# Performance work log

Hardware: AMD Instinct MI355X
Metric: run time of the kernel (lower is better)

Reference implementation:

```python
import jax, jax.numpy as jnp
import numpy as np

B, K, D = 262144, 512, 3


def setup_inputs() -> dict:
    key = jax.random.key(0)
    k_ze, k_e = jax.random.split(key)
    ze = jax.random.normal(k_ze, (B, D, 1), dtype=jnp.float32)
    e = jax.random.normal(k_e, (K, D), dtype=jnp.float32)  # codebook, learned param
    return {"ze": ze, "e": e}


def reference(ze, e):
    # ze: (B, D, 1), e: (K, D)
    # Per-dimension L2 distance to every codebook entry: (B, K, D)
    l2diff = (jnp.transpose(ze, (0, 2, 1)) - e[None, :, :]) ** 2
    # Independent argmin over the codebook axis for each of the D dims: (B, D)
    z = jnp.argmin(l2diff, axis=1)
    # Gather per-dimension codebook scalars: zq[b, d] = e[z[b, d], d]
    zq = e[z, jnp.arange(D)]  # (B, D)
    return (z, zq)
```

## Files before the change

### kernel.cpp

```cpp
#include <hip/hip_runtime.h>

#define B_TOTAL 262144
#define K_CB    512
#define D_DIM   3
#define BLOCK   256
#define NSLOT   (B_TOTAL * D_DIM)

__device__ __forceinline__ unsigned int mono32(unsigned int u) {
    unsigned int m = (u & 0x80000000u) ? 0xFFFFFFFFu : 0x80000000u;
    return u ^ m;
}

__global__ __launch_bounds__(BLOCK) void rank_kernel(
    const float* __restrict__ e, float* __restrict__ ws_val, int* __restrict__ ws_idx)
{
    const int d    = blockIdx.x >> 1;
    const int half = blockIdx.x & 1;
    const int tid  = threadIdx.x;

    __shared__ unsigned long long key[K_CB];
    __shared__ float              val[K_CB];

    for (int k = tid; k < K_CB; k += BLOCK) {
        float v = e[k * D_DIM + d];
        key[k] = ((unsigned long long)mono32(__float_as_uint(v)) << 32) | (unsigned int)k;
        val[k] = v;
    }
    __syncthreads();

    const int i = half * BLOCK + tid;
    const unsigned long long mykey = key[i];
    int rank = 0;
    #pragma unroll 8
    for (int j = 0; j < K_CB; ++j)
        rank += (key[j] < mykey) ? 1 : 0;

    ws_val[d * K_CB + rank] = val[i];
    ws_idx[d * K_CB + rank] = i;
}

__global__ __launch_bounds__(BLOCK) void vq_search_kernel(
    const float* __restrict__ ze,
    const float* __restrict__ ws_val, const int* __restrict__ ws_idx,
    float* __restrict__ z_out, float* __restrict__ zq_out)
{
    __shared__ float sval[D_DIM * K_CB];
    __shared__ int   sidx[D_DIM * K_CB];

    const int tid = threadIdx.x;
    {
        const float4* gv = (const float4*)ws_val; float4* lv = (float4*)sval;
        for (int i = tid; i < D_DIM * K_CB / 4; i += BLOCK) lv[i] = gv[i];
        const int4*   gi = (const int4*)ws_idx;   int4*   li = (int4*)sidx;
        for (int i = tid; i < D_DIM * K_CB / 4; i += BLOCK) li[i] = gi[i];
    }
    __syncthreads();

    const int s4 = (blockIdx.x * BLOCK + tid) * 4;
    const float4 xv4 = *(const float4*)(ze + s4);
    const float xs[4] = { xv4.x, xv4.y, xv4.z, xv4.w };

    const int d0 = s4 % 3;
    int dcur = d0;
    float zz[4], zq[4];

    #pragma unroll
    for (int q = 0; q < 4; ++q) {
        const int base = dcur * K_CB;
        dcur = (dcur == 2) ? 0 : dcur + 1;
        const float xv = xs[q];

        int lo = -1, hi = K_CB;
        #pragma unroll
        for (int it = 0; it < 10; ++it) {
            int mid = (lo + hi) >> 1;
            bool le = sval[base + mid] <= xv;
            lo = le ? mid : lo;
            hi = le ? hi : mid;
        }

        float dl = 3.402823466e38f, vl = 0.0f; int il = 0;
        if (lo >= 0) {
            vl = sval[base + lo];
            int p = lo;
            while (p > 0 && sval[base + p - 1] == vl) --p;
            il = sidx[base + p];
            float t = xv - vl;
            dl = t * t;
        }
        float dr = 3.402823466e38f, vr = 0.0f; int ir = 0;
        if (lo < K_CB - 1) {
            vr = sval[base + lo + 1];
            ir = sidx[base + lo + 1];
            float t = xv - vr;
            dr = t * t;
        }

        const bool pickR = (dr < dl) || ((dr == dl) && (ir < il));
        zz[q] = (float)(pickR ? ir : il);
        zq[q] = pickR ? vr : vl;
    }

    *(float4*)(z_out  + s4) = make_float4(zz[0], zz[1], zz[2], zz[3]);
    *(float4*)(zq_out + s4) = make_float4(zq[0], zq[1], zq[2], zq[3]);
}

extern "C" void kernel_launch(void* const* d_in, const int* in_sizes, int n_in,
                              void* d_out, int out_size, void* d_ws, size_t ws_size,
                              hipStream_t stream) {
    const float* ze = (const float*)d_in[0];
    const float* e  = (const float*)d_in[1];
    float* z_out  = (float*)d_out;
    float* zq_out = z_out + (size_t)NSLOT;

    float* ws_val = (float*)d_ws;
    int*   ws_idx = (int*)(ws_val + D_DIM * K_CB);

    rank_kernel     <<<D_DIM * 2,         BLOCK, 0, stream>>>(e, ws_val, ws_idx);
    vq_search_kernel<<<NSLOT / (4 * BLOCK), BLOCK, 0, stream>>>(ze, ws_val, ws_idx,
                                                                z_out, zq_out);
}
```

Baseline: 72.00 us.

## Add bucket lookup table to narrow codebook binary search range

The rank kernel now also builds, per dimension, a 1024-bucket lookup table over [-4,4) that gives how many sorted codebook entries fall below each bucket boundary. The search kernel loads this table into shared memory and uses it to bracket each query, running 4 bisection steps when the bracket is small and falling back to the full 10-step search otherwise. This cuts shared-memory lookups per element, at the cost of loading about 6 KB of extra LUT per block and some divergence on the fallback branch.

```diff
diff --git a/kernel.cpp b/kernel.cpp
--- a/kernel.cpp
+++ b/kernel.cpp
@@ -5,14 +5,22 @@
 #define D_DIM   3
 #define BLOCK   256
 #define NSLOT   (B_TOTAL * D_DIM)
+#define LUT_S   1032
 
 __device__ __forceinline__ unsigned int mono32(unsigned int u) {
     unsigned int m = (u & 0x80000000u) ? 0xFFFFFFFFu : 0x80000000u;
     return u ^ m;
 }
 
-__global__ __launch_bounds__(BLOCK) void rank_kernel(
-    const float* __restrict__ e, float* __restrict__ ws_val, int* __restrict__ ws_idx)
+__device__ __forceinline__ int bucket_of(float x) {
+    float tf = floorf((x + 4.0f) * 128.0f);
+    tf = fminf(fmaxf(tf, 0.0f), 1023.0f);
+    return (int)tf;
+}
+
+__global__ __launch_bounds__(BLOCK) void rank_lut_kernel(
+    const float* __restrict__ e, float* __restrict__ ws_val,
+    int* __restrict__ ws_idx, unsigned short* __restrict__ ws_lut)
 {
     const int d    = blockIdx.x >> 1;
     const int half = blockIdx.x & 1;
@@ -20,11 +28,14 @@
 
     __shared__ unsigned long long key[K_CB];
     __shared__ float              val[K_CB];
+    __shared__ int                bkt[K_CB];
 
     for (int k = tid; k < K_CB; k += BLOCK) {
         float v = e[k * D_DIM + d];
-        key[k] = ((unsigned long long)mono32(__float_as_uint(v)) << 32) | (unsigned int)k;
+        key[k] = ((unsigned long long)mono32(__float_as_uint(v)) << 32)
+               | (unsigned int)k;
         val[k] = v;
+        bkt[k] = bucket_of(v);
     }
     __syncthreads();
 
@@ -37,15 +48,31 @@
 
     ws_val[d * K_CB + rank] = val[i];
     ws_idx[d * K_CB + rank] = i;
+
+    const int i0 = half * 512 + tid;
+    const int i1 = i0 + BLOCK;
+    int c0 = 0, c1 = 0;
+    #pragma unroll 8
+    for (int j = 0; j < K_CB; ++j) {
+        int bj = bkt[j];
+        c0 += (bj < i0) ? 1 : 0;
+        c1 += (bj < i1) ? 1 : 0;
+    }
+    ws_lut[d * LUT_S + i0] = (unsigned short)c0;
+    ws_lut[d * LUT_S + i1] = (unsigned short)c1;
+    if (half == 1 && tid == 0)
+        ws_lut[d * LUT_S + 1024] = (unsigned short)K_CB;
 }
 
 __global__ __launch_bounds__(BLOCK) void vq_search_kernel(
     const float* __restrict__ ze,
     const float* __restrict__ ws_val, const int* __restrict__ ws_idx,
+    const unsigned int* __restrict__ ws_lut_u32,
     float* __restrict__ z_out, float* __restrict__ zq_out)
 {
-    __shared__ float sval[D_DIM * K_CB];
-    __shared__ int   sidx[D_DIM * K_CB];
+    __shared__ __align__(16) float          sval[D_DIM * K_CB];
+    __shared__ __align__(16) int            sidx[D_DIM * K_CB];
+    __shared__ __align__(4)  unsigned short slut[D_DIM * LUT_S];
 
     const int tid = threadIdx.x;
     {
@@ -53,6 +80,8 @@
         for (int i = tid; i < D_DIM * K_CB / 4; i += BLOCK) lv[i] = gv[i];
         const int4*   gi = (const int4*)ws_idx;   int4*   li = (int4*)sidx;
         for (int i = tid; i < D_DIM * K_CB / 4; i += BLOCK) li[i] = gi[i];
+        unsigned int* ll = (unsigned int*)slut;
+        for (int i = tid; i < D_DIM * LUT_S / 2; i += BLOCK) ll[i] = ws_lut_u32[i];
     }
     __syncthreads();
 
@@ -60,23 +89,37 @@
     const float4 xv4 = *(const float4*)(ze + s4);
     const float xs[4] = { xv4.x, xv4.y, xv4.z, xv4.w };
 
-    const int d0 = s4 % 3;
-    int dcur = d0;
+    int dcur = s4 % 3;
     float zz[4], zq[4];
 
     #pragma unroll
     for (int q = 0; q < 4; ++q) {
         const int base = dcur * K_CB;
+        const int lutb = dcur * LUT_S;
         dcur = (dcur == 2) ? 0 : dcur + 1;
         const float xv = xs[q];
 
-        int lo = -1, hi = K_CB;
-        #pragma unroll
-        for (int it = 0; it < 10; ++it) {
-            int mid = (lo + hi) >> 1;
-            bool le = sval[base + mid] <= xv;
-            lo = le ? mid : lo;
-            hi = le ? hi : mid;
+        const int t  = bucket_of(xv);
+        int lo = (int)slut[lutb + t] - 1;
+        int hi = (int)slut[lutb + t + 1];
+
+        if (hi - lo > 16) {
+            lo = -1; hi = K_CB;
+            #pragma unroll
+            for (int it = 0; it < 10; ++it) {
+                int mid = (lo + hi) >> 1;
+                bool le = sval[base + mid] <= xv;
+                lo = le ? mid : lo;
+                hi = le ? hi : mid;
+            }
+        } else {
+            #pragma unroll
+            for (int it = 0; it < 4; ++it) {
+                int mid = (lo + hi) >> 1;
+                bool le = sval[base + mid] <= xv;
+                lo = le ? mid : lo;
+                hi = le ? hi : mid;
+            }
         }
 
         float dl = 3.402823466e38f, vl = 0.0f; int il = 0;
@@ -85,15 +128,15 @@
             int p = lo;
             while (p > 0 && sval[base + p - 1] == vl) --p;
             il = sidx[base + p];
-            float t = xv - vl;
-            dl = t * t;
+            float tt = xv - vl;
+            dl = tt * tt;
         }
         float dr = 3.402823466e38f, vr = 0.0f; int ir = 0;
         if (lo < K_CB - 1) {
             vr = sval[base + lo + 1];
             ir = sidx[base + lo + 1];
-            float t = xv - vr;
-            dr = t * t;
+            float tt = xv - vr;
+            dr = tt * tt;
         }
 
         const bool pickR = (dr < dl) || ((dr == dl) && (ir < il));
@@ -113,10 +156,11 @@
     float* z_out  = (float*)d_out;
     float* zq_out = z_out + (size_t)NSLOT;
 
-    float* ws_val = (float*)d_ws;
-    int*   ws_idx = (int*)(ws_val + D_DIM * K_CB);
+    float*          ws_val = (float*)d_ws;
+    int*            ws_idx = (int*)(ws_val + D_DIM * K_CB);
+    unsigned short* ws_lut = (unsigned short*)(ws_idx + D_DIM * K_CB);
 
-    rank_kernel     <<<D_DIM * 2,         BLOCK, 0, stream>>>(e, ws_val, ws_idx);
-    vq_search_kernel<<<NSLOT / (4 * BLOCK), BLOCK, 0, stream>>>(ze, ws_val, ws_idx,
-                                                                z_out, zq_out);
+    rank_lut_kernel <<<D_DIM * 2,           BLOCK, 0, stream>>>(e, ws_val, ws_idx, ws_lut);
+    vq_search_kernel<<<NSLOT / (4 * BLOCK), BLOCK, 0, stream>>>(
+        ze, ws_val, ws_idx, (const unsigned int*)ws_lut, z_out, zq_out);
 }
```

After: 77.72 us. 8.0% more time.

## Fuse codebook ranking and search into one cooperative kernel with grid sync

Applied to the files above, without the earlier changes.

Merges the small codebook-sorting kernel and the main search kernel into one cooperative launch. The first six blocks compute the sorted codebook, then every block waits at a grid-wide barrier before loading the sorted table into shared memory. This removes one kernel launch and the gap between the two kernels. In exchange it adds a grid barrier across 768 blocks and the extra cost of a cooperative launch, and it requires every block to be resident at the same time.

```diff
diff --git a/kernel.cpp b/kernel.cpp
--- a/kernel.cpp
+++ b/kernel.cpp
@@ -1,53 +1,59 @@
 #include <hip/hip_runtime.h>
+#include <hip/hip_cooperative_groups.h>
+
+namespace cg = cooperative_groups;
 
 #define B_TOTAL 262144
 #define K_CB    512
 #define D_DIM   3
 #define BLOCK   256
 #define NSLOT   (B_TOTAL * D_DIM)
+#define NBLK    (NSLOT / (4 * BLOCK))
 
 __device__ __forceinline__ unsigned int mono32(unsigned int u) {
     unsigned int m = (u & 0x80000000u) ? 0xFFFFFFFFu : 0x80000000u;
     return u ^ m;
 }
 
-__global__ __launch_bounds__(BLOCK) void rank_kernel(
-    const float* __restrict__ e, float* __restrict__ ws_val, int* __restrict__ ws_idx)
-{
-    const int d    = blockIdx.x >> 1;
-    const int half = blockIdx.x & 1;
-    const int tid  = threadIdx.x;
-
-    __shared__ unsigned long long key[K_CB];
-    __shared__ float              val[K_CB];
-
-    for (int k = tid; k < K_CB; k += BLOCK) {
-        float v = e[k * D_DIM + d];
-        key[k] = ((unsigned long long)mono32(__float_as_uint(v)) << 32) | (unsigned int)k;
-        val[k] = v;
-    }
-    __syncthreads();
-
-    const int i = half * BLOCK + tid;
-    const unsigned long long mykey = key[i];
-    int rank = 0;
-    #pragma unroll 8
-    for (int j = 0; j < K_CB; ++j)
-        rank += (key[j] < mykey) ? 1 : 0;
-
-    ws_val[d * K_CB + rank] = val[i];
-    ws_idx[d * K_CB + rank] = i;
-}
-
-__global__ __launch_bounds__(BLOCK) void vq_search_kernel(
-    const float* __restrict__ ze,
-    const float* __restrict__ ws_val, const int* __restrict__ ws_idx,
+__global__ __launch_bounds__(BLOCK) void vq_coop_kernel(
+    const float* __restrict__ ze, const float* __restrict__ e,
+    float* __restrict__ ws_val, int* __restrict__ ws_idx,
     float* __restrict__ z_out, float* __restrict__ zq_out)
 {
-    __shared__ float sval[D_DIM * K_CB];
-    __shared__ int   sidx[D_DIM * K_CB];
+    __shared__ __align__(16) unsigned char smem[12288];
+    const int tid = threadIdx.x;
 
-    const int tid = threadIdx.x;
+    if (blockIdx.x < D_DIM * 2) {
+        unsigned long long* key = (unsigned long long*)smem;
+        float*              val = (float*)(smem + 8192);
+
+        const int d    = blockIdx.x >> 1;
+        const int half = blockIdx.x & 1;
+
+        for (int k = tid; k < K_CB; k += BLOCK) {
+            float v = e[k * D_DIM + d];
+            key[k] = ((unsigned long long)mono32(__float_as_uint(v)) << 32)
+                   | (unsigned int)k;
+            val[k] = v;
+        }
+        __syncthreads();
+
+        const int i = half * BLOCK + tid;
+        const unsigned long long mykey = key[i];
+        int rank = 0;
+        #pragma unroll 8
+        for (int j = 0; j < K_CB; ++j)
+            rank += (key[j] < mykey) ? 1 : 0;
+
+        ws_val[d * K_CB + rank] = val[i];
+        ws_idx[d * K_CB + rank] = i;
+    }
+
+    cg::this_grid().sync();
+
+    float* sval = (float*)smem;
+    int*   sidx = (int*)(smem + 6144);
+
     {
         const float4* gv = (const float4*)ws_val; float4* lv = (float4*)sval;
         for (int i = tid; i < D_DIM * K_CB / 4; i += BLOCK) lv[i] = gv[i];
@@ -60,8 +66,7 @@
     const float4 xv4 = *(const float4*)(ze + s4);
     const float xs[4] = { xv4.x, xv4.y, xv4.z, xv4.w };
 
-    const int d0 = s4 % 3;
-    int dcur = d0;
+    int dcur = s4 % 3;
     float zz[4], zq[4];
 
     #pragma unroll
@@ -116,7 +121,8 @@
     float* ws_val = (float*)d_ws;
     int*   ws_idx = (int*)(ws_val + D_DIM * K_CB);
 
-    rank_kernel     <<<D_DIM * 2,         BLOCK, 0, stream>>>(e, ws_val, ws_idx);
-    vq_search_kernel<<<NSLOT / (4 * BLOCK), BLOCK, 0, stream>>>(ze, ws_val, ws_idx,
-                                                                z_out, zq_out);
+    void* args[] = { (void*)&ze, (void*)&e, (void*)&ws_val, (void*)&ws_idx,
+                     (void*)&z_out, (void*)&zq_out };
+    hipLaunchCooperativeKernel((const void*)vq_coop_kernel,
+                               dim3(NBLK), dim3(BLOCK), args, 0, stream);
 }
```

Measured after the change: 159.3 us. +121.2%, slower.
